# Performance work log

Hardware: AMD Instinct MI355X
Metric: run time of the kernel (lower is better)

## Reference

```python
import jax, jax.numpy as jnp
import numpy as np

N_NODES = 100000
N_EDGES = 1600000
D_IN, D_HID, N_CLS = 256, 128, 47


def setup_inputs() -> dict:
    key = jax.random.key(0)
    k = jax.random.split(key, 5)
    x = jax.random.normal(k[0], (N_NODES, D_IN), dtype=jnp.float32)
    edge_index = jax.random.randint(k[1], (2, N_EDGES), 0, N_NODES, dtype=jnp.int64)
    W1 = jax.random.normal(k[2], (D_IN, D_HID), dtype=jnp.float32) * 0.05
    b1 = jnp.zeros((D_HID,), dtype=jnp.float32)
    W2 = jax.random.normal(k[3], (D_HID, N_CLS), dtype=jnp.float32) * 0.05
    b2 = jnp.zeros((N_CLS,), dtype=jnp.float32)
    return {"x": x, "edge_index": edge_index, "W1": W1, "b1": b1, "W2": W2, "b2": b2}


def _gcn_conv(x, W, b, src, dst, norm, n):
    # PyG GCNConv: linear transform, normalized scatter-add aggregation, bias after
    h = x @ W                                   # [N, D_out]
    msg = h[src] * norm[:, None]                # gather over edges [E', D_out]
    agg = jax.ops.segment_sum(msg, dst, num_segments=n)
    return agg + b


def reference(x, edge_index, W1, b1, W2, b2):
    n = x.shape[0]
    loop = jnp.arange(n, dtype=edge_index.dtype)
    src = jnp.concatenate([edge_index[0], loop])  # add self-loops
    dst = jnp.concatenate([edge_index[1], loop])
    # symmetric normalization D^-1/2 (A+I) D^-1/2 (degree = in-degree incl. self-loop)
    deg = jax.ops.segment_sum(jnp.ones_like(dst, dtype=x.dtype), dst, num_segments=n)
    dinv = jnp.where(deg > 0, jax.lax.rsqrt(deg), 0.0)
    norm = dinv[src] * dinv[dst]                 # [E']
    h1 = jax.nn.relu(_gcn_conv(x, W1, b1, src, dst, norm, n))
    # dropout with training=False is identity
    out = _gcn_conv(h1, W2, b2, src, dst, norm, n)
    return out
```

## Files before the change

### kernel.cpp

```cpp
#include <hip/hip_runtime.h>
#include <hip/hip_bf16.h>

#define DIN 256
#define DHID 128
#define NCLS 47
#define BSHIFT 9
#define BNODES 512
#define NPART 256
#define BCAPS 9216
#define CHUNKE 6400

typedef __attribute__((ext_vector_type(8))) short short8;
typedef __attribute__((ext_vector_type(4))) float f32x4;

__device__ __forceinline__ short f2bf(float f) {
    __bf16 b = (__bf16)f;
    return __builtin_bit_cast(short, b);
}
__device__ __forceinline__ float bfu(unsigned int u) {
    return __uint_as_float(u << 16);
}
__device__ __forceinline__ float bfh(unsigned int u) {
    return __uint_as_float(u & 0xffff0000u);
}
__device__ __forceinline__ unsigned int pack2(float lo, float hi) {
    return (unsigned int)(unsigned short)f2bf(lo)
         | ((unsigned int)(unsigned short)f2bf(hi) << 16);
}
__device__ __forceinline__ void add8(float* a, uint4 v) {
    a[0] += bfu(v.x); a[1] += bfh(v.x);
    a[2] += bfu(v.y); a[3] += bfh(v.y);
    a[4] += bfu(v.z); a[5] += bfh(v.z);
    a[6] += bfu(v.w); a[7] += bfh(v.w);
}

__global__ __launch_bounds__(256) void k_prep_hist(const float* __restrict__ W1,
                                                   const float* __restrict__ W2,
                                                   short* __restrict__ W1s,
                                                   short* __restrict__ W2s,
                                                   const int* __restrict__ dst,
                                                   int* __restrict__ ghist,
                                                   int E, int NB, int chunk) {
    __shared__ int lh[256];
    int blk = blockIdx.x, t = threadIdx.x;
    if (blk < 16) {
        int tid = blk * 256 + t;
        int frag = tid >> 6, lane = tid & 63;
        int kt = frag >> 3, nt = frag & 7;
        int quad = lane >> 4, col = lane & 15;
        #pragma unroll
        for (int j = 0; j < 8; ++j) {
            int k = kt * 32 + quad * 8 + j;
            W1s[(size_t)tid * 8 + j] = f2bf(W1[k * DHID + nt * 16 + col]);
        }
    } else if (blk < 20) {
        int tid = (blk - 16) * 256 + t;
        int frag = tid >> 6, lane = tid & 63;
        int kt = frag >> 2, nt = frag & 3;
        int quad = lane >> 4, col = lane & 15;
        int c = nt * 16 + col;
        #pragma unroll
        for (int j = 0; j < 8; ++j) {
            int k = kt * 32 + quad * 8 + j;
            float v = (c < NCLS) ? W2[k * NCLS + c] : 0.0f;
            W2s[(size_t)tid * 8 + j] = f2bf(v);
        }
    } else {
        int p = blk - 20;
        for (int i = t; i < NB; i += 256) lh[i] = 0;
        __syncthreads();
        int lo = p * chunk, hi = min(E, lo + chunk);
        for (int i = lo + t; i < hi; i += 256)
            atomicAdd(&lh[dst[i] >> BSHIFT], 1);
        __syncthreads();
        for (int i = t; i < NB; i += 256) ghist[p * NB + i] = lh[i];
    }
}

__global__ __launch_bounds__(256) void k_colscan(const int* __restrict__ ghist,
                                                 int* __restrict__ goff,
                                                 int* __restrict__ btot, int NB) {
    __shared__ int wsum[4];
    int b = blockIdx.x, t = threadIdx.x;
    int v = ghist[t * NB + b];
    int incl = v;
    int lane = t & 63, w = t >> 6;
    #pragma unroll
    for (int off = 1; off < 64; off <<= 1) {
        int u = __shfl_up(incl, off, 64);
        if (lane >= off) incl += u;
    }
    if (lane == 63) wsum[w] = incl;
    __syncthreads();
    int wadd = 0;
    for (int i = 0; i < w; ++i) wadd += wsum[i];
    goff[t * NB + b] = wadd + incl - v;
    if (t == 255) btot[b] = wadd + incl;
}

__device__ __forceinline__ void scan_btot(const int* __restrict__ btot, int NB,
                                          int* lbase, int* wsum) {
    int t = threadIdx.x;
    int v = (t < NB) ? btot[t] : 0;
    int incl = v;
    int lane = t & 63, w = t >> 6;
    #pragma unroll
    for (int off = 1; off < 64; off <<= 1) {
        int u = __shfl_up(incl, off, 64);
        if (lane >= off) incl += u;
    }
    if (lane == 63) wsum[w] = incl;
    __syncthreads();
    int wadd = 0;
    for (int i = 0; i < w; ++i) wadd += wsum[i];
    lbase[t] = wadd + incl - v;
    __syncthreads();
}

__global__ __launch_bounds__(256) void k_scatter(const int* __restrict__ src,
                                                 const int* __restrict__ dst,
                                                 const int* __restrict__ ghist,
                                                 const int* __restrict__ goff,
                                                 const int* __restrict__ btot,
                                                 unsigned int* __restrict__ bbuf,
                                                 int E, int NB, int chunk) {
    __shared__ unsigned int stage[CHUNKE];
    __shared__ int sdest[CHUNKE];
    __shared__ int lcur[256];
    __shared__ int gdst[256];
    __shared__ int wsum[4];

    int blk = blockIdx.x, t = threadIdx.x;

    scan_btot(btot, NB, gdst, wsum);

    int v = (t < NB) ? ghist[blk * NB + t] : 0;
    {
        int incl = v;
        int lane = t & 63, w = t >> 6;
        #pragma unroll
        for (int off = 1; off < 64; off <<= 1) {
            int u = __shfl_up(incl, off, 64);
            if (lane >= off) incl += u;
        }
        if (lane == 63) wsum[w] = incl;
        __syncthreads();
        int wadd = 0;
        for (int i = 0; i < w; ++i) wadd += wsum[i];
        int ex = wadd + incl - v;
        lcur[t] = ex;
        if (t < NB) gdst[t] += goff[blk * NB + t] - ex;
    }
    __syncthreads();

    int lo = blk * chunk, hi = min(E, lo + chunk), cnt = hi - lo;
    for (int i = lo + t; i < hi; i += 256) {
        int d = dst[i];
        int b = d >> BSHIFT;
        int slot = atomicAdd(&lcur[b], 1);
        stage[slot] = (unsigned int)src[i] | ((unsigned int)(d & (BNODES - 1)) << 17);
        sdest[slot] = gdst[b] + slot;
    }
    __syncthreads();
    for (int i = t; i < cnt; i += 256)
        bbuf[sdest[i]] = stage[i];
}

__global__ __launch_bounds__(256) void k_bsort(const int* __restrict__ btot,
                                               unsigned int* __restrict__ bbuf,
                                               int* __restrict__ degi,
                                               int* __restrict__ beg,
                                               float* __restrict__ dinv, int n, int NB) {
    __shared__ unsigned int stage[BCAPS];
    __shared__ int hist[BNODES];
    __shared__ int cur[BNODES];
    __shared__ int lbase[256];
    __shared__ int wsum[4];

    int b = blockIdx.x, t = threadIdx.x;
    scan_btot(btot, NB, lbase, wsum);
    int cnt = min(btot[b], BCAPS);
    int gbase = lbase[b];
    int node0 = b << BSHIFT;

    if (t < 128) { ((int2*)hist)[t] = (int2){0, 0}; ((int2*)hist)[t + 128] = (int2){0, 0}; }
    __syncthreads();

    for (int i = t; i < cnt; i += 256) {
        unsigned int p = bbuf[gbase + i];
        stage[i] = p;
        atomicAdd(&hist[p >> 17], 1);
    }
    __syncthreads();

    int v0 = hist[2 * t], v1 = hist[2 * t + 1];
    int s = v0 + v1;
    int incl = s;
    int lane = t & 63, w = t >> 6;
    #pragma unroll
    for (int off = 1; off < 64; off <<= 1) {
        int u = __shfl_up(incl, off, 64);
        if (lane >= off) incl += u;
    }
    if (lane == 63) wsum[w] = incl;
    __syncthreads();
    int wadd = 0;
    for (int i = 0; i < w; ++i) wadd += wsum[i];
    int ex = wadd + incl - s;
    cur[2 * t] = ex;
    cur[2 * t + 1] = ex + v0;
    int nodeA = node0 + 2 * t, nodeB = node0 + 2 * t + 1;
    if (nodeA < n) {
        degi[nodeA] = v0;
        beg[nodeA]  = gbase + ex;
        dinv[nodeA] = rsqrtf((float)(v0 + 1));
    }
    if (nodeB < n) {
        degi[nodeB] = v1;
        beg[nodeB]  = gbase + ex + v0;
        dinv[nodeB] = rsqrtf((float)(v1 + 1));
    }
    __syncthreads();

    for (int i = t; i < cnt; i += 256) {
        unsigned int p = stage[i];
        int slot = atomicAdd(&cur[p >> 17], 1);
        bbuf[gbase + slot] = p & 0x1FFFFu;
    }
}

__global__ __launch_bounds__(256) void k_gemm1_mfma(const float* __restrict__ x,
                                                    const short* __restrict__ W1s,
                                                    const float* __restrict__ dinv,
                                                    short* __restrict__ hb, int n) {
    __shared__ short lw[32768];
    {
        const uint4* g = (const uint4*)W1s;
        uint4* l = (uint4*)lw;
        for (int i = threadIdx.x; i < 4096; i += 256) l[i] = g[i];
    }
    __syncthreads();

    int wave = threadIdx.x >> 6, lane = threadIdx.x & 63;
    int quad = lane >> 4, lrow = lane & 15;
    long long rowbase = (long long)blockIdx.x * 128 + wave * 32;

    f32x4 acc[2][8];
    #pragma unroll
    for (int rt = 0; rt < 2; ++rt)
        #pragma unroll
        for (int nt = 0; nt < 8; ++nt) acc[rt][nt] = (f32x4){0.f, 0.f, 0.f, 0.f};

    const short8* lf = (const short8*)lw;

    #pragma unroll
    for (int kt = 0; kt < 8; ++kt) {
        int k0 = kt * 32 + quad * 8;
        short8 a[2];
        #pragma unroll
        for (int rt = 0; rt < 2; ++rt) {
            long long row = rowbase + rt * 16 + lrow;
            float4 v0 = {0.f,0.f,0.f,0.f}, v1 = {0.f,0.f,0.f,0.f};
            if (row < n) {
                const float* xp = x + row * DIN + k0;
                v0 = *(const float4*)xp;
                v1 = *(const float4*)(xp + 4);
            }
            short8 av;
            av[0] = f2bf(v0.x); av[1] = f2bf(v0.y); av[2] = f2bf(v0.z); av[3] = f2bf(v0.w);
            av[4] = f2bf(v1.x); av[5] = f2bf(v1.y); av[6] = f2bf(v1.z); av[7] = f2bf(v1.w);
            a[rt] = av;
        }
        #pragma unroll
        for (int nt = 0; nt < 8; ++nt) {
            short8 b = lf[(kt * 8 + nt) * 64 + lane];
            acc[0][nt] = __builtin_amdgcn_mfma_f32_16x16x32_bf16(a[0], b, acc[0][nt], 0, 0, 0);
            acc[1][nt] = __builtin_amdgcn_mfma_f32_16x16x32_bf16(a[1], b, acc[1][nt], 0, 0, 0);
        }
    }
    float dvv[2][4];
    #pragma unroll
    for (int rt = 0; rt < 2; ++rt)
        #pragma unroll
        for (int r = 0; r < 4; ++r) {
            long long row = rowbase + rt * 16 + quad * 4 + r;
            dvv[rt][r] = (row < n) ? dinv[row] : 0.f;
        }
    #pragma unroll
    for (int rt = 0; rt < 2; ++rt)
        #pragma unroll
        for (int nt = 0; nt < 8; ++nt)
            #pragma unroll
            for (int r = 0; r < 4; ++r) {
                long long row = rowbase + rt * 16 + quad * 4 + r;
                if (row < n) hb[row * DHID + nt * 16 + lrow] = f2bf(acc[rt][nt][r] * dvv[rt][r]);
            }
}

__global__ __launch_bounds__(256) void k_gather1(const int* __restrict__ beg,
                          const int* __restrict__ degi,
                          const int* __restrict__ ssrc, const float* __restrict__ dinv,
                          const uint4* __restrict__ hb4, const float* __restrict__ b1,
                          uint4* __restrict__ h1u4, int n) {
    int node = blockIdx.x * 4 + (threadIdx.x >> 6);
    int t = threadIdx.x & 63;
    if (node >= n) return;
    int cnt = degi[node];
    int bg  = beg[node];
    int grp = t >> 4, sub = t & 15;

    float a[8] = {0.f,0.f,0.f,0.f,0.f,0.f,0.f,0.f};
    int k = 0;
    for (; k + 16 <= cnt; k += 16) {
        int s[4];
        #pragma unroll
        for (int q = 0; q < 4; ++q) s[q] = ssrc[bg + k + q * 4 + grp];
        uint4 v[4];
        #pragma unroll
        for (int q = 0; q < 4; ++q) v[q] = hb4[(size_t)s[q] * 16 + sub];
        #pragma unroll
        for (int q = 0; q < 4; ++q) add8(a, v[q]);
    }
    for (; k + 8 <= cnt; k += 8) {
        int s0 = ssrc[bg + k + grp], s1 = ssrc[bg + k + 4 + grp];
        uint4 v0 = hb4[(size_t)s0 * 16 + sub];
        uint4 v1 = hb4[(size_t)s1 * 16 + sub];
        add8(a, v0); add8(a, v1);
    }
    for (; k < cnt; k += 4) {
        int idx = k + grp;
        if (idx < cnt) {
            int s = ssrc[bg + idx];
            add8(a, hb4[(size_t)s * 16 + sub]);
        }
    }
    if (grp == 0) add8(a, hb4[(size_t)node * 16 + sub]);

    #pragma unroll
    for (int j = 0; j < 8; ++j) {
        a[j] += __shfl_xor(a[j], 16);
        a[j] += __shfl_xor(a[j], 32);
    }

    if (grp == 0) {
        float di = dinv[node];
        float4 bA = ((const float4*)b1)[sub * 2];
        float4 bB = ((const float4*)b1)[sub * 2 + 1];
        float v0 = fmaxf(di * a[0] + bA.x, 0.f);
        float v1 = fmaxf(di * a[1] + bA.y, 0.f);
        float v2 = fmaxf(di * a[2] + bA.z, 0.f);
        float v3 = fmaxf(di * a[3] + bA.w, 0.f);
        float v4 = fmaxf(di * a[4] + bB.x, 0.f);
        float v5 = fmaxf(di * a[5] + bB.y, 0.f);
        float v6 = fmaxf(di * a[6] + bB.z, 0.f);
        float v7 = fmaxf(di * a[7] + bB.w, 0.f);
        uint4 o;
        o.x = pack2(v0, v1);
        o.y = pack2(v2, v3);
        o.z = pack2(v4, v5);
        o.w = pack2(v6, v7);
        h1u4[(size_t)node * 16 + sub] = o;
    }
}

__global__ __launch_bounds__(256) void k_gemm2_mfma(const short* __restrict__ h1b,
                                                    const short* __restrict__ W2s,
                                                    const float* __restrict__ dinv,
                                                    short* __restrict__ h2b, int n) {
    __shared__ short lw[8192];
    {
        const uint4* g = (const uint4*)W2s;
        uint4* l = (uint4*)lw;
        for (int i = threadIdx.x; i < 1024; i += 256) l[i] = g[i];
    }
    __syncthreads();

    int wave = threadIdx.x >> 6, lane = threadIdx.x & 63;
    int quad = lane >> 4, lrow = lane & 15;
    long long row0 = (long long)blockIdx.x * 64 + wave * 16;

    f32x4 acc[4];
    #pragma unroll
    for (int nt = 0; nt < 4; ++nt) acc[nt] = (f32x4){0.f, 0.f, 0.f, 0.f};

    const short8* lf = (const short8*)lw;

    #pragma unroll
    for (int kt = 0; kt < 4; ++kt) {
        long long row = row0 + lrow;
        short8 a = (short8){0,0,0,0,0,0,0,0};
        if (row < n) a = *(const short8*)(h1b + row * DHID + kt * 32 + quad * 8);
        #pragma unroll
        for (int nt = 0; nt < 4; ++nt)
            acc[nt] = __builtin_amdgcn_mfma_f32_16x16x32_bf16(a, lf[(kt * 4 + nt) * 64 + lane], acc[nt], 0, 0, 0);
    }
    float dvv[4];
    #pragma unroll
    for (int r = 0; r < 4; ++r) {
        long long row = row0 + quad * 4 + r;
        dvv[r] = (row < n) ? dinv[row] : 0.f;
    }
    #pragma unroll
    for (int nt = 0; nt < 4; ++nt)
        #pragma unroll
        for (int r = 0; r < 4; ++r) {
            long long row = row0 + quad * 4 + r;
            if (row < n) h2b[row * 64 + nt * 16 + lrow] = f2bf(acc[nt][r] * dvv[r]);
        }
}

__global__ __launch_bounds__(256) void k_gather2(const int* __restrict__ beg,
                          const int* __restrict__ degi,
                          const int* __restrict__ ssrc, const float* __restrict__ dinv,
                          const uint4* __restrict__ h2b4, const float* __restrict__ b2,
                          float* __restrict__ out, int n) {
    int node = blockIdx.x * 4 + (threadIdx.x >> 6);
    int t = threadIdx.x & 63;
    if (node >= n) return;
    int cnt = degi[node];
    int bg  = beg[node];
    int grp = t >> 3, sub = t & 7;

    float a[8] = {0.f,0.f,0.f,0.f,0.f,0.f,0.f,0.f};
    int k = 0;
    for (; k + 16 <= cnt; k += 16) {
        int s0 = ssrc[bg + k + grp], s1 = ssrc[bg + k + 8 + grp];
        uint4 v0 = h2b4[(size_t)s0 * 8 + sub];
        uint4 v1 = h2b4[(size_t)s1 * 8 + sub];
        add8(a, v0); add8(a, v1);
    }
    for (; k < cnt; k += 8) {
        int idx = k + grp;
        if (idx < cnt) {
            int s = ssrc[bg + idx];
            add8(a, h2b4[(size_t)s * 8 + sub]);
        }
    }
    if (grp == 0) add8(a, h2b4[(size_t)node * 8 + sub]);

    #pragma unroll
    for (int j = 0; j < 8; ++j) {
        a[j] += __shfl_xor(a[j], 8);
        a[j] += __shfl_xor(a[j], 16);
        a[j] += __shfl_xor(a[j], 32);
    }

    if (grp == 0) {
        float di = dinv[node];
        #pragma unroll
        for (int j = 0; j < 8; ++j) {
            int c = sub * 8 + j;
            if (c < NCLS) out[(size_t)node * NCLS + c] = di * a[j] + b2[c];
        }
    }
}

extern "C" void kernel_launch(void* const* d_in, const int* in_sizes, int n_in,
                              void* d_out, int out_size, void* d_ws, size_t ws_size,
                              hipStream_t stream) {
    const float* x  = (const float*)d_in[0];
    const int*   ei = (const int*)d_in[1];
    const float* W1 = (const float*)d_in[2];
    const float* b1 = (const float*)d_in[3];
    const float* W2 = (const float*)d_in[4];
    const float* b2 = (const float*)d_in[5];

    const int n = in_sizes[0] / DIN;
    const int E = in_sizes[1] / 2;
    const int* src = ei;
    const int* dst = ei + E;
    float* out = (float*)d_out;

    const int NB = (n + BNODES - 1) >> BSHIFT;
    const int chunk = (E + NPART - 1) / NPART;

    char* w = (char*)d_ws;
    int*   ghist = (int*)w;                    w += (size_t)NPART * NB * 4;
    int*   goff  = (int*)w;                    w += (size_t)NPART * NB * 4;
    int*   btot  = (int*)w;                    w += ((size_t)NB * 4 + 15) & ~15ull;
    int*   degi  = (int*)w;                    w += (size_t)n * 4;
    int*   beg   = (int*)w;                    w += (size_t)n * 4;
    float* dinv  = (float*)w;                  w += (size_t)n * 4;
    short* W1s   = (short*)w;                  w += (size_t)32768 * 2;
    short* W2s   = (short*)w;                  w += (size_t)8192 * 2;
    unsigned int* bbuf = (unsigned int*)w;     w += (size_t)E * 4;
    short* hb    = (short*)w;                  w += (size_t)n * DHID * 2;
    short* h1b   = (short*)w;                  w += (size_t)n * DHID * 2;
    short* h2b   = (short*)w;                  w += (size_t)n * 64 * 2;

    k_prep_hist<<<20 + NPART, 256, 0, stream>>>(W1, W2, W1s, W2s, dst, ghist, E, NB, chunk);
    k_colscan<<<NB, 256, 0, stream>>>(ghist, goff, btot, NB);
    k_scatter<<<NPART, 256, 0, stream>>>(src, dst, ghist, goff, btot, bbuf, E, NB, chunk);
    k_bsort<<<NB, 256, 0, stream>>>(btot, bbuf, degi, beg, dinv, n, NB);

    k_gemm1_mfma<<<(n + 127) / 128, 256, 0, stream>>>(x, W1s, dinv, hb, n);
    k_gather1<<<(n + 3) / 4, 256, 0, stream>>>(beg, degi, (const int*)bbuf, dinv,
                                               (const uint4*)hb, b1,
                                               (uint4*)h1b, n);

    k_gemm2_mfma<<<(n + 63) / 64, 256, 0, stream>>>(h1b, W2s, dinv, h2b, n);
    k_gather2<<<(n + 3) / 4, 256, 0, stream>>>(beg, degi, (const int*)bbuf, dinv,
                                               (const uint4*)h2b, b2, out, n);
}
```

Before: 417.8 us.

## Fuse colscan into scatter, merge bsort with GEMM1, one-node-per-group gathers

Folds the column-scan kernel into the scatter kernel: each block rereads the whole histogram to get its prefix and the bucket totals. The bucket sort and the first GEMM are merged into one launch, with separate block ranges running independent work concurrently. Because the GEMM can no longer depend on dinv, source normalisation moves into the gathers, which now weight each neighbour by dinv[src]. The gathers also give each node a 16- or 8-lane group instead of a full wave, removing the cross-lane reductions. This cuts kernel launches and idle time, but adds redundant histogram reads per scatter block and more dinv gathers per edge.

```diff
diff --git a/kernel.cpp b/kernel.cpp
--- a/kernel.cpp
+++ b/kernel.cpp
@@ -27,11 +27,11 @@
     return (unsigned int)(unsigned short)f2bf(lo)
          | ((unsigned int)(unsigned short)f2bf(hi) << 16);
 }
-__device__ __forceinline__ void add8(float* a, uint4 v) {
-    a[0] += bfu(v.x); a[1] += bfh(v.x);
-    a[2] += bfu(v.y); a[3] += bfh(v.y);
-    a[4] += bfu(v.z); a[5] += bfh(v.z);
-    a[6] += bfu(v.w); a[7] += bfh(v.w);
+__device__ __forceinline__ void fma8(float* a, uint4 v, float d) {
+    a[0] += d * bfu(v.x); a[1] += d * bfh(v.x);
+    a[2] += d * bfu(v.y); a[3] += d * bfh(v.y);
+    a[4] += d * bfu(v.z); a[5] += d * bfh(v.z);
+    a[6] += d * bfu(v.w); a[7] += d * bfh(v.w);
 }
 
 __global__ __launch_bounds__(256) void k_prep_hist(const float* __restrict__ W1,
@@ -77,51 +77,10 @@
     }
 }
 
-__global__ __launch_bounds__(256) void k_colscan(const int* __restrict__ ghist,
-                                                 int* __restrict__ goff,
-                                                 int* __restrict__ btot, int NB) {
-    __shared__ int wsum[4];
-    int b = blockIdx.x, t = threadIdx.x;
-    int v = ghist[t * NB + b];
-    int incl = v;
-    int lane = t & 63, w = t >> 6;
-    #pragma unroll
-    for (int off = 1; off < 64; off <<= 1) {
-        int u = __shfl_up(incl, off, 64);
-        if (lane >= off) incl += u;
-    }
-    if (lane == 63) wsum[w] = incl;
-    __syncthreads();
-    int wadd = 0;
-    for (int i = 0; i < w; ++i) wadd += wsum[i];
-    goff[t * NB + b] = wadd + incl - v;
-    if (t == 255) btot[b] = wadd + incl;
-}
-
-__device__ __forceinline__ void scan_btot(const int* __restrict__ btot, int NB,
-                                          int* lbase, int* wsum) {
-    int t = threadIdx.x;
-    int v = (t < NB) ? btot[t] : 0;
-    int incl = v;
-    int lane = t & 63, w = t >> 6;
-    #pragma unroll
-    for (int off = 1; off < 64; off <<= 1) {
-        int u = __shfl_up(incl, off, 64);
-        if (lane >= off) incl += u;
-    }
-    if (lane == 63) wsum[w] = incl;
-    __syncthreads();
-    int wadd = 0;
-    for (int i = 0; i < w; ++i) wadd += wsum[i];
-    lbase[t] = wadd + incl - v;
-    __syncthreads();
-}
-
 __global__ __launch_bounds__(256) void k_scatter(const int* __restrict__ src,
                                                  const int* __restrict__ dst,
                                                  const int* __restrict__ ghist,
-                                                 const int* __restrict__ goff,
-                                                 const int* __restrict__ btot,
+                                                 int* __restrict__ btot,
                                                  unsigned int* __restrict__ bbuf,
                                                  int E, int NB, int chunk) {
     __shared__ unsigned int stage[CHUNKE];
@@ -132,25 +91,45 @@
 
     int blk = blockIdx.x, t = threadIdx.x;
 
-    scan_btot(btot, NB, gdst, wsum);
-
-    int v = (t < NB) ? ghist[blk * NB + t] : 0;
-    {
-        int incl = v;
-        int lane = t & 63, w = t >> 6;
-        #pragma unroll
-        for (int off = 1; off < 64; off <<= 1) {
-            int u = __shfl_up(incl, off, 64);
-            if (lane >= off) incl += u;
-        }
-        if (lane == 63) wsum[w] = incl;
-        __syncthreads();
-        int wadd = 0;
-        for (int i = 0; i < w; ++i) wadd += wsum[i];
-        int ex = wadd + incl - v;
-        lcur[t] = ex;
-        if (t < NB) gdst[t] += goff[blk * NB + t] - ex;
-    }
+    int tot = 0, pref = 0;
+    if (t < NB) {
+        #pragma unroll 8
+        for (int p = 0; p < NPART; ++p) {
+            int v = ghist[p * NB + t];
+            tot += v;
+            if (p < blk) pref += v;
+        }
+    }
+    int mine = (t < NB) ? ghist[blk * NB + t] : 0;
+    if (blk == 0 && t < NB) btot[t] = tot;
+
+    int lane = t & 63, w = t >> 6;
+    int incl = tot;
+    #pragma unroll
+    for (int off = 1; off < 64; off <<= 1) {
+        int u = __shfl_up(incl, off, 64);
+        if (lane >= off) incl += u;
+    }
+    if (lane == 63) wsum[w] = incl;
+    __syncthreads();
+    int wadd = 0;
+    for (int i = 0; i < w; ++i) wadd += wsum[i];
+    int bbase = wadd + incl - tot;
+    __syncthreads();
+    incl = mine;
+    #pragma unroll
+    for (int off = 1; off < 64; off <<= 1) {
+        int u = __shfl_up(incl, off, 64);
+        if (lane >= off) incl += u;
+    }
+    if (lane == 63) wsum[w] = incl;
+    __syncthreads();
+    wadd = 0;
+    for (int i = 0; i < w; ++i) wadd += wsum[i];
+    int ex = wadd + incl - mine;
+
+    lcur[t] = ex;
+    gdst[t] = bbase + pref - ex;
     __syncthreads();
 
     int lo = blk * chunk, hi = min(E, lo + chunk), cnt = hi - lo;
@@ -166,36 +145,11 @@
         bbuf[sdest[i]] = stage[i];
 }
 
-__global__ __launch_bounds__(256) void k_bsort(const int* __restrict__ btot,
-                                               unsigned int* __restrict__ bbuf,
-                                               int* __restrict__ degi,
-                                               int* __restrict__ beg,
-                                               float* __restrict__ dinv, int n, int NB) {
-    __shared__ unsigned int stage[BCAPS];
-    __shared__ int hist[BNODES];
-    __shared__ int cur[BNODES];
-    __shared__ int lbase[256];
-    __shared__ int wsum[4];
-
-    int b = blockIdx.x, t = threadIdx.x;
-    scan_btot(btot, NB, lbase, wsum);
-    int cnt = min(btot[b], BCAPS);
-    int gbase = lbase[b];
-    int node0 = b << BSHIFT;
-
-    if (t < 128) { ((int2*)hist)[t] = (int2){0, 0}; ((int2*)hist)[t + 128] = (int2){0, 0}; }
-    __syncthreads();
-
-    for (int i = t; i < cnt; i += 256) {
-        unsigned int p = bbuf[gbase + i];
-        stage[i] = p;
-        atomicAdd(&hist[p >> 17], 1);
-    }
-    __syncthreads();
-
-    int v0 = hist[2 * t], v1 = hist[2 * t + 1];
-    int s = v0 + v1;
-    int incl = s;
+__device__ __forceinline__ void scan_btot(const int* __restrict__ btot, int NB,
+                                          int* lbase, int* wsum) {
+    int t = threadIdx.x;
+    int v = (t < NB) ? btot[t] : 0;
+    int incl = v;
     int lane = t & 63, w = t >> 6;
     #pragma unroll
     for (int off = 1; off < 64; off <<= 1) {
@@ -206,95 +160,136 @@
     __syncthreads();
     int wadd = 0;
     for (int i = 0; i < w; ++i) wadd += wsum[i];
-    int ex = wadd + incl - s;
-    cur[2 * t] = ex;
-    cur[2 * t + 1] = ex + v0;
-    int nodeA = node0 + 2 * t, nodeB = node0 + 2 * t + 1;
-    if (nodeA < n) {
-        degi[nodeA] = v0;
-        beg[nodeA]  = gbase + ex;
-        dinv[nodeA] = rsqrtf((float)(v0 + 1));
-    }
-    if (nodeB < n) {
-        degi[nodeB] = v1;
-        beg[nodeB]  = gbase + ex + v0;
-        dinv[nodeB] = rsqrtf((float)(v1 + 1));
-    }
-    __syncthreads();
-
-    for (int i = t; i < cnt; i += 256) {
-        unsigned int p = stage[i];
-        int slot = atomicAdd(&cur[p >> 17], 1);
-        bbuf[gbase + slot] = p & 0x1FFFFu;
-    }
-}
-
-__global__ __launch_bounds__(256) void k_gemm1_mfma(const float* __restrict__ x,
-                                                    const short* __restrict__ W1s,
-                                                    const float* __restrict__ dinv,
-                                                    short* __restrict__ hb, int n) {
-    __shared__ short lw[32768];
-    {
-        const uint4* g = (const uint4*)W1s;
-        uint4* l = (uint4*)lw;
-        for (int i = threadIdx.x; i < 4096; i += 256) l[i] = g[i];
-    }
-    __syncthreads();
-
-    int wave = threadIdx.x >> 6, lane = threadIdx.x & 63;
-    int quad = lane >> 4, lrow = lane & 15;
-    long long rowbase = (long long)blockIdx.x * 128 + wave * 32;
-
-    f32x4 acc[2][8];
-    #pragma unroll
-    for (int rt = 0; rt < 2; ++rt)
-        #pragma unroll
-        for (int nt = 0; nt < 8; ++nt) acc[rt][nt] = (f32x4){0.f, 0.f, 0.f, 0.f};
-
-    const short8* lf = (const short8*)lw;
-
-    #pragma unroll
-    for (int kt = 0; kt < 8; ++kt) {
-        int k0 = kt * 32 + quad * 8;
-        short8 a[2];
-        #pragma unroll
-        for (int rt = 0; rt < 2; ++rt) {
-            long long row = rowbase + rt * 16 + lrow;
-            float4 v0 = {0.f,0.f,0.f,0.f}, v1 = {0.f,0.f,0.f,0.f};
-            if (row < n) {
-                const float* xp = x + row * DIN + k0;
-                v0 = *(const float4*)xp;
-                v1 = *(const float4*)(xp + 4);
+    lbase[t] = wadd + incl - v;
+    __syncthreads();
+}
+
+__global__ __launch_bounds__(256) void k_bsort_gemm1(const int* __restrict__ btot,
+                                                     unsigned int* __restrict__ bbuf,
+                                                     int* __restrict__ degi,
+                                                     int* __restrict__ beg,
+                                                     float* __restrict__ dinv,
+                                                     int n, int NB,
+                                                     const float* __restrict__ x,
+                                                     const short* __restrict__ W1s,
+                                                     short* __restrict__ hb) {
+    __shared__ __align__(16) char smem[65536];
+    int blk = blockIdx.x, t = threadIdx.x;
+
+    if (blk < NB) {
+        unsigned int* stage = (unsigned int*)smem;
+        int* hist  = (int*)(smem + 36864);
+        int* cur   = (int*)(smem + 38912);
+        int* lbase = (int*)(smem + 40960);
+        int* wsum  = (int*)(smem + 41984);
+
+        int b = blk;
+        scan_btot(btot, NB, lbase, wsum);
+        int cnt = min(btot[b], BCAPS);
+        int gbase = lbase[b];
+        int node0 = b << BSHIFT;
+
+        if (t < 128) { ((int2*)hist)[t] = (int2){0, 0}; ((int2*)hist)[t + 128] = (int2){0, 0}; }
+        __syncthreads();
+
+        for (int i = t; i < cnt; i += 256) {
+            unsigned int p = bbuf[gbase + i];
+            stage[i] = p;
+            atomicAdd(&hist[p >> 17], 1);
+        }
+        __syncthreads();
+
+        int v0 = hist[2 * t], v1 = hist[2 * t + 1];
+        int s = v0 + v1;
+        int incl = s;
+        int lane = t & 63, w = t >> 6;
+        #pragma unroll
+        for (int off = 1; off < 64; off <<= 1) {
+            int u = __shfl_up(incl, off, 64);
+            if (lane >= off) incl += u;
+        }
+        if (lane == 63) wsum[w] = incl;
+        __syncthreads();
+        int wadd = 0;
+        for (int i = 0; i < w; ++i) wadd += wsum[i];
+        int ex = wadd + incl - s;
+        cur[2 * t] = ex;
+        cur[2 * t + 1] = ex + v0;
+        int nodeA = node0 + 2 * t, nodeB = node0 + 2 * t + 1;
+        if (nodeA < n) {
+            degi[nodeA] = v0;
+            beg[nodeA]  = gbase + ex;
+            dinv[nodeA] = rsqrtf((float)(v0 + 1));
+        }
+        if (nodeB < n) {
+            degi[nodeB] = v1;
+            beg[nodeB]  = gbase + ex + v0;
+            dinv[nodeB] = rsqrtf((float)(v1 + 1));
+        }
+        __syncthreads();
+
+        for (int i = t; i < cnt; i += 256) {
+            unsigned int p = stage[i];
+            int slot = atomicAdd(&cur[p >> 17], 1);
+            bbuf[gbase + slot] = p & 0x1FFFFu;
+        }
+    } else {
+        short* lw = (short*)smem;
+        {
+            const uint4* g = (const uint4*)W1s;
+            uint4* l = (uint4*)lw;
+            for (int i = t; i < 4096; i += 256) l[i] = g[i];
+        }
+        __syncthreads();
+
+        int bid = blk - NB;
+        int wave = t >> 6, lane = t & 63;
+        int quad = lane >> 4, lrow = lane & 15;
+        long long rowbase = (long long)bid * 128 + wave * 32;
+
+        f32x4 acc[2][8];
+        #pragma unroll
+        for (int rt = 0; rt < 2; ++rt)
+            #pragma unroll
+            for (int nt = 0; nt < 8; ++nt) acc[rt][nt] = (f32x4){0.f, 0.f, 0.f, 0.f};
+
+        const short8* lf = (const short8*)lw;
+
+        #pragma unroll
+        for (int kt = 0; kt < 8; ++kt) {
+            int k0 = kt * 32 + quad * 8;
+            short8 a[2];
+            #pragma unroll
+            for (int rt = 0; rt < 2; ++rt) {
+                long long row = rowbase + rt * 16 + lrow;
+                float4 v0 = {0.f,0.f,0.f,0.f}, v1 = {0.f,0.f,0.f,0.f};
+                if (row < n) {
+                    const float* xp = x + row * DIN + k0;
+                    v0 = *(const float4*)xp;
+                    v1 = *(const float4*)(xp + 4);
+                }
+                short8 av;
+                av[0] = f2bf(v0.x); av[1] = f2bf(v0.y); av[2] = f2bf(v0.z); av[3] = f2bf(v0.w);
+                av[4] = f2bf(v1.x); av[5] = f2bf(v1.y); av[6] = f2bf(v1.z); av[7] = f2bf(v1.w);
+                a[rt] = av;
             }
-            short8 av;
-            av[0] = f2bf(v0.x); av[1] = f2bf(v0.y); av[2] = f2bf(v0.z); av[3] = f2bf(v0.w);
-            av[4] = f2bf(v1.x); av[5] = f2bf(v1.y); av[6] = f2bf(v1.z); av[7] = f2bf(v1.w);
-            a[rt] = av;
-        }
-        #pragma unroll
-        for (int nt = 0; nt < 8; ++nt) {
-            short8 b = lf[(kt * 8 + nt) * 64 + lane];
-            acc[0][nt] = __builtin_amdgcn_mfma_f32_16x16x32_bf16(a[0], b, acc[0][nt], 0, 0, 0);
-            acc[1][nt] = __builtin_amdgcn_mfma_f32_16x16x32_bf16(a[1], b, acc[1][nt], 0, 0, 0);
-        }
-    }
-    float dvv[2][4];
-    #pragma unroll
-    for (int rt = 0; rt < 2; ++rt)
-        #pragma unroll
-        for (int r = 0; r < 4; ++r) {
-            long long row = rowbase + rt * 16 + quad * 4 + r;
-            dvv[rt][r] = (row < n) ? dinv[row] : 0.f;
-        }
-    #pragma unroll
-    for (int rt = 0; rt < 2; ++rt)
-        #pragma unroll
-        for (int nt = 0; nt < 8; ++nt)
             #pragma unroll
-            for (int r = 0; r < 4; ++r) {
-                long long row = rowbase + rt * 16 + quad * 4 + r;
-                if (row < n) hb[row * DHID + nt * 16 + lrow] = f2bf(acc[rt][nt][r] * dvv[rt][r]);
+            for (int nt = 0; nt < 8; ++nt) {
+                short8 b = lf[(kt * 8 + nt) * 64 + lane];
+                acc[0][nt] = __builtin_amdgcn_mfma_f32_16x16x32_bf16(a[0], b, acc[0][nt], 0, 0, 0);
+                acc[1][nt] = __builtin_amdgcn_mfma_f32_16x16x32_bf16(a[1], b, acc[1][nt], 0, 0, 0);
             }
+        }
+        #pragma unroll
+        for (int rt = 0; rt < 2; ++rt)
+            #pragma unroll
+            for (int nt = 0; nt < 8; ++nt)
+                #pragma unroll
+                for (int r = 0; r < 4; ++r) {
+                    long long row = rowbase + rt * 16 + quad * 4 + r;
+                    if (row < n) hb[row * DHID + nt * 16 + lrow] = f2bf(acc[rt][nt][r]);
+                }
+    }
 }
 
 __global__ __launch_bounds__(256) void k_gather1(const int* __restrict__ beg,
@@ -302,70 +297,56 @@
                           const int* __restrict__ ssrc, const float* __restrict__ dinv,
                           const uint4* __restrict__ hb4, const float* __restrict__ b1,
                           uint4* __restrict__ h1u4, int n) {
-    int node = blockIdx.x * 4 + (threadIdx.x >> 6);
     int t = threadIdx.x & 63;
+    int wv = threadIdx.x >> 6;
+    int grp = t >> 4, sub = t & 15;
+    int node = blockIdx.x * 16 + wv * 4 + grp;
     if (node >= n) return;
     int cnt = degi[node];
     int bg  = beg[node];
-    int grp = t >> 4, sub = t & 15;
 
     float a[8] = {0.f,0.f,0.f,0.f,0.f,0.f,0.f,0.f};
     int k = 0;
-    for (; k + 16 <= cnt; k += 16) {
-        int s[4];
-        #pragma unroll
-        for (int q = 0; q < 4; ++q) s[q] = ssrc[bg + k + q * 4 + grp];
-        uint4 v[4];
-        #pragma unroll
-        for (int q = 0; q < 4; ++q) v[q] = hb4[(size_t)s[q] * 16 + sub];
-        #pragma unroll
-        for (int q = 0; q < 4; ++q) add8(a, v[q]);
-    }
     for (; k + 8 <= cnt; k += 8) {
-        int s0 = ssrc[bg + k + grp], s1 = ssrc[bg + k + 4 + grp];
-        uint4 v0 = hb4[(size_t)s0 * 16 + sub];
-        uint4 v1 = hb4[(size_t)s1 * 16 + sub];
-        add8(a, v0); add8(a, v1);
-    }
-    for (; k < cnt; k += 4) {
-        int idx = k + grp;
+        int s[8];
+        #pragma unroll
+        for (int q = 0; q < 8; ++q) s[q] = ssrc[bg + k + q];
+        float dv[8]; uint4 v[8];
+        #pragma unroll
+        for (int q = 0; q < 8; ++q) { dv[q] = dinv[s[q]]; v[q] = hb4[(size_t)s[q] * 16 + sub]; }
+        #pragma unroll
+        for (int q = 0; q < 8; ++q) fma8(a, v[q], dv[q]);
+    }
+    #pragma unroll
+    for (int q = 0; q < 8; ++q) {
+        int idx = k + q;
         if (idx < cnt) {
             int s = ssrc[bg + idx];
-            add8(a, hb4[(size_t)s * 16 + sub]);
-        }
-    }
-    if (grp == 0) add8(a, hb4[(size_t)node * 16 + sub]);
-
-    #pragma unroll
-    for (int j = 0; j < 8; ++j) {
-        a[j] += __shfl_xor(a[j], 16);
-        a[j] += __shfl_xor(a[j], 32);
-    }
-
-    if (grp == 0) {
-        float di = dinv[node];
-        float4 bA = ((const float4*)b1)[sub * 2];
-        float4 bB = ((const float4*)b1)[sub * 2 + 1];
-        float v0 = fmaxf(di * a[0] + bA.x, 0.f);
-        float v1 = fmaxf(di * a[1] + bA.y, 0.f);
-        float v2 = fmaxf(di * a[2] + bA.z, 0.f);
-        float v3 = fmaxf(di * a[3] + bA.w, 0.f);
-        float v4 = fmaxf(di * a[4] + bB.x, 0.f);
-        float v5 = fmaxf(di * a[5] + bB.y, 0.f);
-        float v6 = fmaxf(di * a[6] + bB.z, 0.f);
-        float v7 = fmaxf(di * a[7] + bB.w, 0.f);
-        uint4 o;
-        o.x = pack2(v0, v1);
-        o.y = pack2(v2, v3);
-        o.z = pack2(v4, v5);
-        o.w = pack2(v6, v7);
-        h1u4[(size_t)node * 16 + sub] = o;
-    }
+            fma8(a, hb4[(size_t)s * 16 + sub], dinv[s]);
+        }
+    }
+    uint4 sv = hb4[(size_t)node * 16 + sub];
+    float di = dinv[node], dd = di * di;
+    float4 bA = ((const float4*)b1)[sub * 2];
+    float4 bB = ((const float4*)b1)[sub * 2 + 1];
+    float v0 = fmaxf(di * a[0] + dd * bfu(sv.x) + bA.x, 0.f);
+    float v1 = fmaxf(di * a[1] + dd * bfh(sv.x) + bA.y, 0.f);
+    float v2 = fmaxf(di * a[2] + dd * bfu(sv.y) + bA.z, 0.f);
+    float v3 = fmaxf(di * a[3] + dd * bfh(sv.y) + bA.w, 0.f);
+    float v4 = fmaxf(di * a[4] + dd * bfu(sv.z) + bB.x, 0.f);
+    float v5 = fmaxf(di * a[5] + dd * bfh(sv.z) + bB.y, 0.f);
+    float v6 = fmaxf(di * a[6] + dd * bfu(sv.w) + bB.z, 0.f);
+    float v7 = fmaxf(di * a[7] + dd * bfh(sv.w) + bB.w, 0.f);
+    uint4 o;
+    o.x = pack2(v0, v1);
+    o.y = pack2(v2, v3);
+    o.z = pack2(v4, v5);
+    o.w = pack2(v6, v7);
+    h1u4[(size_t)node * 16 + sub] = o;
 }
 
 __global__ __launch_bounds__(256) void k_gemm2_mfma(const short* __restrict__ h1b,
                                                     const short* __restrict__ W2s,
-                                                    const float* __restrict__ dinv,
                                                     short* __restrict__ h2b, int n) {
     __shared__ short lw[8192];
     {
@@ -394,18 +375,12 @@
         for (int nt = 0; nt < 4; ++nt)
             acc[nt] = __builtin_amdgcn_mfma_f32_16x16x32_bf16(a, lf[(kt * 4 + nt) * 64 + lane], acc[nt], 0, 0, 0);
     }
-    float dvv[4];
-    #pragma unroll
-    for (int r = 0; r < 4; ++r) {
-        long long row = row0 + quad * 4 + r;
-        dvv[r] = (row < n) ? dinv[row] : 0.f;
-    }
     #pragma unroll
     for (int nt = 0; nt < 4; ++nt)
         #pragma unroll
         for (int r = 0; r < 4; ++r) {
             long long row = row0 + quad * 4 + r;
-            if (row < n) h2b[row * 64 + nt * 16 + lrow] = f2bf(acc[nt][r] * dvv[r]);
+            if (row < n) h2b[row * 64 + nt * 16 + lrow] = f2bf(acc[nt][r]);
         }
 }
 
@@ -414,44 +389,42 @@
                           const int* __restrict__ ssrc, const float* __restrict__ dinv,
                           const uint4* __restrict__ h2b4, const float* __restrict__ b2,
                           float* __restrict__ out, int n) {
-    int node = blockIdx.x * 4 + (threadIdx.x >> 6);
     int t = threadIdx.x & 63;
+    int wv = threadIdx.x >> 6;
+    int grp = t >> 3, sub = t & 7;
+    int node = blockIdx.x * 32 + wv * 8 + grp;
     if (node >= n) return;
     int cnt = degi[node];
     int bg  = beg[node];
-    int grp = t >> 3, sub = t & 7;
 
     float a[8] = {0.f,0.f,0.f,0.f,0.f,0.f,0.f,0.f};
     int k = 0;
-    for (; k + 16 <= cnt; k += 16) {
-        int s0 = ssrc[bg + k + grp], s1 = ssrc[bg + k + 8 + grp];
-        uint4 v0 = h2b4[(size_t)s0 * 8 + sub];
-        uint4 v1 = h2b4[(size_t)s1 * 8 + sub];
-        add8(a, v0); add8(a, v1);
-    }
-    for (; k < cnt; k += 8) {
-        int idx = k + grp;
+    for (; k + 8 <= cnt; k += 8) {
+        int s[8];
+        #pragma unroll
+        for (int q = 0; q < 8; ++q) s[q] = ssrc[bg + k + q];
+        float dv[8]; uint4 v[8];
+        #pragma unroll
+        for (int q = 0; q < 8; ++q) { dv[q] = dinv[s[q]]; v[q] = h2b4[(size_t)s[q] * 8 + sub]; }
+        #pragma unroll
+        for (int q = 0; q < 8; ++q) fma8(a, v[q], dv[q]);
+    }
+    #pragma unroll
+    for (int q = 0; q < 8; ++q) {
+        int idx = k + q;
         if (idx < cnt) {
             int s = ssrc[bg + idx];
-            add8(a, h2b4[(size_t)s * 8 + sub]);
-        }
-    }
-    if (grp == 0) add8(a, h2b4[(size_t)node * 8 + sub]);
-
+            fma8(a, h2b4[(size_t)s * 8 + sub], dinv[s]);
+        }
+    }
+    uint4 sv = h2b4[(size_t)node * 8 + sub];
+    float di = dinv[node], dd = di * di;
+    float sf[8] = { bfu(sv.x), bfh(sv.x), bfu(sv.y), bfh(sv.y),
+                    bfu(sv.z), bfh(sv.z), bfu(sv.w), bfh(sv.w) };
     #pragma unroll
     for (int j = 0; j < 8; ++j) {
-        a[j] += __shfl_xor(a[j], 8);
-        a[j] += __shfl_xor(a[j], 16);
-        a[j] += __shfl_xor(a[j], 32);
-    }
-
-    if (grp == 0) {
-        float di = dinv[node];
-        #pragma unroll
-        for (int j = 0; j < 8; ++j) {
-            int c = sub * 8 + j;
-            if (c < NCLS) out[(size_t)node * NCLS + c] = di * a[j] + b2[c];
-        }
+        int c = sub * 8 + j;
+        if (c < NCLS) out[(size_t)node * NCLS + c] = di * a[j] + dd * sf[j] + b2[c];
     }
 }
 
@@ -476,7 +449,6 @@
 
     char* w = (char*)d_ws;
     int*   ghist = (int*)w;                    w += (size_t)NPART * NB * 4;
-    int*   goff  = (int*)w;                    w += (size_t)NPART * NB * 4;
     int*   btot  = (int*)w;                    w += ((size_t)NB * 4 + 15) & ~15ull;
     int*   degi  = (int*)w;                    w += (size_t)n * 4;
     int*   beg   = (int*)w;                    w += (size_t)n * 4;
@@ -489,16 +461,16 @@
     short* h2b   = (short*)w;                  w += (size_t)n * 64 * 2;
 
     k_prep_hist<<<20 + NPART, 256, 0, stream>>>(W1, W2, W1s, W2s, dst, ghist, E, NB, chunk);
-    k_colscan<<<NB, 256, 0, stream>>>(ghist, goff, btot, NB);
-    k_scatter<<<NPART, 256, 0, stream>>>(src, dst, ghist, goff, btot, bbuf, E, NB, chunk);
-    k_bsort<<<NB, 256, 0, stream>>>(btot, bbuf, degi, beg, dinv, n, NB);
-
-    k_gemm1_mfma<<<(n + 127) / 128, 256, 0, stream>>>(x, W1s, dinv, hb, n);
-    k_gather1<<<(n + 3) / 4, 256, 0, stream>>>(beg, degi, (const int*)bbuf, dinv,
-                                               (const uint4*)hb, b1,
-                                               (uint4*)h1b, n);
-
-    k_gemm2_mfma<<<(n + 63) / 64, 256, 0, stream>>>(h1b, W2s, dinv, h2b, n);
-    k_gather2<<<(n + 3) / 4, 256, 0, stream>>>(beg, degi, (const int*)bbuf, dinv,
-                                               (const uint4*)h2b, b2, out, n);
-}
+    k_scatter<<<NPART, 256, 0, stream>>>(src, dst, ghist, btot, bbuf, E, NB, chunk);
+
+    k_bsort_gemm1<<<NB + (n + 127) / 128, 256, 0, stream>>>(btot, bbuf, degi, beg, dinv,
+                                                            n, NB, x, W1s, hb);
+
+    k_gather1<<<(n + 15) / 16, 256, 0, stream>>>(beg, degi, (const int*)bbuf, dinv,
+                                                 (const uint4*)hb, b1,
+                                                 (uint4*)h1b, n);
+
+    k_gemm2_mfma<<<(n + 63) / 64, 256, 0, stream>>>(h1b, W2s, h2b, n);
+    k_gather2<<<(n + 31) / 32, 256, 0, stream>>>(beg, degi, (const int*)bbuf, dinv,
+                                                 (const uint4*)h2b, b2, out, n);
+}
```

Result: faster. 408.8 us (-2.2%).
